# Optimization experiments

Hardware: AMD Instinct MI355X
Metric: run time of the kernel (lower is better)

The kernel has to match this reference:

```python
import jax, jax.numpy as jnp
import numpy as np

MAXDISP = 48  # init kwarg
KS = list(range(3, 12))  # window sizes 3..11 -> channel prefixes k*k (9..121)


def setup_inputs() -> dict:
    key = jax.random.key(0)
    k1, k2 = jax.random.split(key)
    B, C, H, W = 2, 121, 128, 256
    x = jax.random.normal(k1, (B, C, H, W), dtype=jnp.float32)
    y = jax.random.normal(k2, (B, C, H, W), dtype=jnp.float32)
    return {"x": x, "y": y}


def reference(x, y):
    # GetCostVolume forward (attack=True branch: mean |x - shifted y| over
    # nested channel prefixes idx=k*k, k=3..11, for each disparity shift).
    # Note: the attack=False branch replaces |x-y| with (x!=y).float(); for
    # continuous random inputs that is identically 1, so we implement the
    # differentiable abs-diff branch, which has identical loop/memory structure.
    B, C, H, W = x.shape
    ksq = jnp.array([k * k for k in KS], dtype=x.dtype)          # (9,) divisors
    prefix_idx = jnp.array([k * k - 1 for k in KS])              # cumsum gather idx
    wpos = jnp.arange(W)

    def body(carry, d):
        # shift y right by d along width; region w<d is masked to zero below,
        # matching cost[..., :d] = 0 from the torch zeros-init.
        y_sh = jnp.roll(y, d, axis=-1)                           # (B,C,H,W)
        diff = jnp.abs(x - y_sh)                                 # (B,C,H,W)
        csum = jnp.cumsum(diff, axis=1)                          # prefix sums over channels
        means = csum[:, prefix_idx] / ksq[:, None, None]         # (B,9,H,W)
        means = jnp.where(wpos >= d, means, jnp.zeros((), x.dtype))
        return carry, means

    _, cost = jax.lax.scan(body, None, jnp.arange(MAXDISP))      # (D,B,9,H,W)
    return jnp.transpose(cost, (1, 2, 0, 3, 4))                  # (B,9,D,H,W)
```

## Files before the change

### kernel.cpp

```cpp
#include <hip/hip_runtime.h>

#define B_ 2
#define C_ 121
#define H_ 128
#define W_ 256
#define D_ 48
#define CT 11
#define NCHUNK 11
#define NT 256
#define NDY 4
#define YROW 312
#define ZS 3

typedef const void __attribute__((address_space(1)))* gas1_t;
typedef void __attribute__((address_space(3)))* las3_t;

__launch_bounds__(NT)
__global__ void cost_volume_kernel(const float* __restrict__ xg,
                                   const float* __restrict__ yg,
                                   float* __restrict__ out)
{
    __shared__ __align__(16) float XLS[2][CT][W_];
    __shared__ __align__(16) float YLS[2][CT][YROW];

    const int t  = threadIdx.x;
    const int h  = blockIdx.x;
    const int b  = blockIdx.y;
    const int z  = blockIdx.z;
    const int wq = t & 63;
    const int wv = t >> 6;
    const int d0 = z * 16 + wv * NDY;

    for (int i = t; i < 2 * CT * 48; i += NT) {
        int nb = i / (CT * 48);
        int r  = i % (CT * 48);
        YLS[nb][r / 48][r % 48] = 0.0f;
    }

    auto stage = [&](int chunk, int nb) {
        for (int i = wv; i < 2 * CT; i += 4) {
            const int cc = i >> 1;
            const int c  = chunk * CT + cc;
            const size_t row = (((size_t)b * C_ + c) * H_ + h) * (size_t)W_;
            if (i & 1) {
                __builtin_amdgcn_global_load_lds((gas1_t)(yg + row + (size_t)wq * 4),
                                                 (las3_t)&YLS[nb][cc][48], 16, 0, 0);
            } else {
                __builtin_amdgcn_global_load_lds((gas1_t)(xg + row + (size_t)wq * 4),
                                                 (las3_t)&XLS[nb][cc][0], 16, 0, 0);
            }
        }
    };

    float acc[NDY][4];
    #pragma unroll
    for (int jd = 0; jd < NDY; ++jd)
        #pragma unroll
        for (int jw = 0; jw < 4; ++jw) acc[jd][jw] = 0.0f;

    stage(0, 0);
    __syncthreads();

    for (int k = 0; k < NCHUNK; ++k) {
        const int cur = k & 1;
        if (k + 1 < NCHUNK) stage(k + 1, cur ^ 1);

        #pragma unroll
        for (int cc = 0; cc < CT; ++cc) {
            const float4 xv = *(const float4*)&XLS[cur][cc][wq * 4];
            const float xvv[4] = {xv.x, xv.y, xv.z, xv.w};

            const int bp = wq * 4 - d0 + 44;
            float yw[8];
            *(float4*)&yw[0] = *(const float4*)&YLS[cur][cc][bp];
            *(float4*)&yw[4] = *(const float4*)&YLS[cur][cc][bp + 4];

            #pragma unroll
            for (int jd = 0; jd < NDY; ++jd)
                #pragma unroll
                for (int jw = 0; jw < 4; ++jw)
                    acc[jd][jw] += __builtin_fabsf(xvv[jw] - yw[4 + jw - jd]);

            #pragma unroll
            for (int bi = 0; bi < 9; ++bi) {
                constexpr int KB[9] = {8, 15, 24, 35, 48, 63, 80, 99, 120};
                const int bc = KB[bi];
                if (k * CT + cc == bc) {
                    const float inv = 1.0f / (float)(bc + 1);
                    const size_t obase = (((size_t)b * 9 + bi) * D_) * (size_t)(H_ * W_)
                                       + (size_t)h * W_ + (size_t)wq * 4;
                    #pragma unroll
                    for (int jd = 0; jd < NDY; ++jd) {
                        const int d = d0 + jd;
                        float4 v;
                        v.x = (wq * 4 + 0 >= d) ? acc[jd][0] * inv : 0.0f;
                        v.y = (wq * 4 + 1 >= d) ? acc[jd][1] * inv : 0.0f;
                        v.z = (wq * 4 + 2 >= d) ? acc[jd][2] * inv : 0.0f;
                        v.w = (wq * 4 + 3 >= d) ? acc[jd][3] * inv : 0.0f;
                        *(float4*)&out[obase + (size_t)d * (H_ * W_)] = v;
                    }
                }
            }
        }
        __syncthreads();
    }
}

extern "C" void kernel_launch(void* const* d_in, const int* in_sizes, int n_in,
                              void* d_out, int out_size, void* d_ws, size_t ws_size,
                              hipStream_t stream)
{
    const float* x = (const float*)d_in[0];
    const float* y = (const float*)d_in[1];
    float* o = (float*)d_out;
    dim3 grid(H_, B_, ZS);
    dim3 block(NT, 1, 1);
    hipLaunchKernelGGL(cost_volume_kernel, grid, block, 0, stream, x, y, o);
}
```

Before: 50.17 us.

## Replace LDS double-buffered staging with direct global loads and nontemporal stores

Removes the shared-memory staging path (async global-to-LDS loads, double buffering, per-chunk barriers) and has each thread read its x and shifted y float4 vectors straight from global memory, relying on L1/L2 cache for the overlapping y windows across waves. Clamped y offsets replace the zero-padded LDS region; values read there are masked out at the store. Output writes become nontemporal stores to avoid polluting cache. This drops barriers and LDS traffic but adds redundant global/cache loads and exposes load latency without explicit prefetch.

```diff
diff --git a/kernel.cpp b/kernel.cpp
--- a/kernel.cpp
+++ b/kernel.cpp
@@ -5,24 +5,17 @@
 #define H_ 128
 #define W_ 256
 #define D_ 48
-#define CT 11
-#define NCHUNK 11
 #define NT 256
 #define NDY 4
-#define YROW 312
 #define ZS 3
 
-typedef const void __attribute__((address_space(1)))* gas1_t;
-typedef void __attribute__((address_space(3)))* las3_t;
+typedef float f32x4 __attribute__((ext_vector_type(4)));
 
 __launch_bounds__(NT)
 __global__ void cost_volume_kernel(const float* __restrict__ xg,
                                    const float* __restrict__ yg,
                                    float* __restrict__ out)
 {
-    __shared__ __align__(16) float XLS[2][CT][W_];
-    __shared__ __align__(16) float YLS[2][CT][YROW];
-
     const int t  = threadIdx.x;
     const int h  = blockIdx.x;
     const int b  = blockIdx.y;
@@ -30,27 +23,18 @@
     const int wq = t & 63;
     const int wv = t >> 6;
     const int d0 = z * 16 + wv * NDY;
+    const int w0 = wq * 4;
 
-    for (int i = t; i < 2 * CT * 48; i += NT) {
-        int nb = i / (CT * 48);
-        int r  = i % (CT * 48);
-        YLS[nb][r / 48][r % 48] = 0.0f;
-    }
+    const int g0 = w0 - d0 - 4;
+    const int gA = g0     > 0 ? g0     : 0;
+    const int gB = g0 + 4 > 0 ? g0 + 4 : 0;
 
-    auto stage = [&](int chunk, int nb) {
-        for (int i = wv; i < 2 * CT; i += 4) {
-            const int cc = i >> 1;
-            const int c  = chunk * CT + cc;
-            const size_t row = (((size_t)b * C_ + c) * H_ + h) * (size_t)W_;
-            if (i & 1) {
-                __builtin_amdgcn_global_load_lds((gas1_t)(yg + row + (size_t)wq * 4),
-                                                 (las3_t)&YLS[nb][cc][48], 16, 0, 0);
-            } else {
-                __builtin_amdgcn_global_load_lds((gas1_t)(xg + row + (size_t)wq * 4),
-                                                 (las3_t)&XLS[nb][cc][0], 16, 0, 0);
-            }
-        }
-    };
+    const size_t row0 = (((size_t)b * C_) * H_ + h) * (size_t)W_;
+    const float* xp = xg + row0 + w0;
+    const float* pA = yg + row0 + gA;
+    const float* pB = yg + row0 + gB;
+
+    constexpr int HW = H_ * W_;
 
     float acc[NDY][4];
     #pragma unroll
@@ -58,23 +42,17 @@
         #pragma unroll
         for (int jw = 0; jw < 4; ++jw) acc[jd][jw] = 0.0f;
 
-    stage(0, 0);
-    __syncthreads();
+    int co = 0;
+    for (int k = 0; k < 11; ++k) {
+        #pragma unroll
+        for (int cc = 0; cc < 11; ++cc) {
+            const f32x4 xv = *(const f32x4*)(xp + co);
+            float yw[8];
+            *(f32x4*)&yw[0] = *(const f32x4*)(pA + co);
+            *(f32x4*)&yw[4] = *(const f32x4*)(pB + co);
+            co += HW;
 
-    for (int k = 0; k < NCHUNK; ++k) {
-        const int cur = k & 1;
-        if (k + 1 < NCHUNK) stage(k + 1, cur ^ 1);
-
-        #pragma unroll
-        for (int cc = 0; cc < CT; ++cc) {
-            const float4 xv = *(const float4*)&XLS[cur][cc][wq * 4];
             const float xvv[4] = {xv.x, xv.y, xv.z, xv.w};
-
-            const int bp = wq * 4 - d0 + 44;
-            float yw[8];
-            *(float4*)&yw[0] = *(const float4*)&YLS[cur][cc][bp];
-            *(float4*)&yw[4] = *(const float4*)&YLS[cur][cc][bp + 4];
-
             #pragma unroll
             for (int jd = 0; jd < NDY; ++jd)
                 #pragma unroll
@@ -85,24 +63,24 @@
             for (int bi = 0; bi < 9; ++bi) {
                 constexpr int KB[9] = {8, 15, 24, 35, 48, 63, 80, 99, 120};
                 const int bc = KB[bi];
-                if (k * CT + cc == bc) {
+                if (k * 11 + cc == bc) {
                     const float inv = 1.0f / (float)(bc + 1);
-                    const size_t obase = (((size_t)b * 9 + bi) * D_) * (size_t)(H_ * W_)
-                                       + (size_t)h * W_ + (size_t)wq * 4;
+                    const size_t obase = (((size_t)b * 9 + bi) * D_) * (size_t)HW
+                                       + (size_t)h * W_ + (size_t)w0;
                     #pragma unroll
                     for (int jd = 0; jd < NDY; ++jd) {
                         const int d = d0 + jd;
-                        float4 v;
-                        v.x = (wq * 4 + 0 >= d) ? acc[jd][0] * inv : 0.0f;
-                        v.y = (wq * 4 + 1 >= d) ? acc[jd][1] * inv : 0.0f;
-                        v.z = (wq * 4 + 2 >= d) ? acc[jd][2] * inv : 0.0f;
-                        v.w = (wq * 4 + 3 >= d) ? acc[jd][3] * inv : 0.0f;
-                        *(float4*)&out[obase + (size_t)d * (H_ * W_)] = v;
+                        f32x4 v;
+                        v.x = (w0 + 0 >= d) ? acc[jd][0] * inv : 0.0f;
+                        v.y = (w0 + 1 >= d) ? acc[jd][1] * inv : 0.0f;
+                        v.z = (w0 + 2 >= d) ? acc[jd][2] * inv : 0.0f;
+                        v.w = (w0 + 3 >= d) ? acc[jd][3] * inv : 0.0f;
+                        __builtin_nontemporal_store(v,
+                            (f32x4*)&out[obase + (size_t)d * HW]);
                     }
                 }
             }
         }
-        __syncthreads();
     }
 }
 
```

New measurement: 65.61 us. 1.31x slower.
